# Optimization experiments

Measured on AMD Instinct MI355X. Metric: run time of the kernel, lower is better.

The kernel has to match this reference:

```python
import jax, jax.numpy as jnp
import numpy as np

QMIN, QMAX = -128, 127  # signed int8 range


def setup_inputs() -> dict:
    key = jax.random.key(0)
    k_x, k_w, k_b = jax.random.split(key, 3)
    N, C_in, H, W = 32, 128, 56, 56
    C_out, kH, kW = 256, 3, 3
    # int8-valued tensors carried as int32 (jax-friendly); values in [-128, 127]
    x = jax.random.randint(k_x, (N, C_in, H, W), 0, 256, dtype=jnp.int32) - 128
    weight = jax.random.randint(k_w, (C_out, C_in, kH, kW), 0, 256, dtype=jnp.int32) - 128
    # int32 bias, already quantized with scale s_in * s_w
    bias = jax.random.randint(k_b, (C_out,), -(2 ** 14), 2 ** 14, dtype=jnp.int32)
    return {
        "x": x,
        "weight": weight,
        "bias": bias,
        "input_scale": jnp.float32(0.02),
        "weight_scale": jnp.float32(0.005),
        "output_scale": jnp.float32(0.05),
        "input_zero_point": jnp.int32(-5),
        "output_zero_point": jnp.int32(3),
    }


def reference(x, weight, bias, input_scale, weight_scale, output_scale,
              input_zero_point, output_zero_point):
    # Dequant-style integer conv: shift input by its zero point (weights are
    # symmetric, zero point 0), accumulate in fp32 (stands in for int32 acc).
    x_f = (x - input_zero_point).astype(jnp.float32)
    w_f = weight.astype(jnp.float32)
    acc = jax.lax.conv_general_dilated(
        x_f, w_f,
        window_strides=(1, 1),
        padding=((1, 1), (1, 1)),
        dimension_numbers=("NCHW", "OIHW", "NCHW"),
    )
    acc = acc + bias.astype(jnp.float32)[None, :, None, None]
    # Requantize: scale fusion + output zero point, round, clamp to int8.
    requant_scale = input_scale * weight_scale / output_scale
    y = acc * requant_scale + output_zero_point.astype(jnp.float32)
    y_q = jnp.clip(jnp.round(y), QMIN, QMAX).astype(jnp.int8)
    return y_q
```

## Files before the change

### kernel.cpp

```cpp
#include <hip/hip_runtime.h>
#include <stdint.h>


#define NB 32
#define CI 128
#define HH 56
#define WW 56
#define CO 256
#define SPA (HH * WW)
#define HP 58
#define WP 64
#define XP2_BYTES (NB * HP * WP * CI)
#define BP_BYTES (9 * 2 * 4 * CO * 16)
#define ABUF (4 * 8192)

typedef int v4i __attribute__((ext_vector_type(4)));

__global__ __launch_bounds__(256) void prep_kernel(
    const int* __restrict__ x, const int* __restrict__ wgt,
    const int* __restrict__ bias, const int* __restrict__ zpi,
    int8_t* __restrict__ xp2, int8_t* __restrict__ bp, int* __restrict__ BG)
{
    __shared__ int sm[1824];
    const int tid = threadIdx.x, bid = blockIdx.x;
    const int zp = *zpi;
    const int zp4 = (zp & 255) * 0x01010101;

    if (bid < HH * NB) {
        const int n = bid / HH, h = bid % HH;
        #pragma unroll
        for (int it = 0; it < 7; ++it) {
            int j = tid + it * 256;
            int ci = j / 14, w4 = j - ci * 14;
            const v4i v = *(const v4i*)(x + ((n * CI + ci) * HH + h) * WW + w4 * 4);
            sm[w4 * 130 + ci] = (v.x & 255) | ((v.y & 255) << 8) |
                                ((v.z & 255) << 16) | (v.w << 24);
        }
        __syncthreads();
        int* od = (int*)xp2 + (n * HP + h + 1) * (WP * CI / 4);
        #pragma unroll
        for (int it = 0; it < 8; ++it) {
            int j = tid + it * 256;
            int widx = j >> 5, ci4 = j & 31;
            int val = zp4;
            if (widx >= 1 && widx <= WW) {
                int w = widx - 1;
                int base = (w >> 2) * 130 + ci4 * 4;
                int sh = (w & 3) * 8;
                val = ((sm[base] >> sh) & 0xff) | (((sm[base+1] >> sh) & 0xff) << 8) |
                      (((sm[base+2] >> sh) & 0xff) << 16) | ((sm[base+3] >> sh) << 24);
            }
            od[j ^ ((widx & 7) << 2)] = val;
        }
    } else if (bid < HH * NB + 2 * NB) {
        const int z = bid - HH * NB;
        const int n = z >> 1, hidx = (z & 1) ? (HP - 1) : 0;
        int* od = (int*)xp2 + (n * HP + hidx) * (WP * CI / 4);
        #pragma unroll
        for (int it = 0; it < 8; ++it) od[tid + it * 256] = zp4;
    } else {
        const int co = bid - (HH * NB + 2 * NB);
        for (int j = tid; j < 1152; j += 256) sm[j] = wgt[co * 1152 + j];
        __syncthreads();
        for (int j = tid; j < 288; j += 256) {
            int j4 = j & 3, q = (j >> 2) & 3, c64 = (j >> 4) & 1, t = j >> 5;
            int ci = c64 * 64 + q * 16 + j4 * 4;
            int b0 = sm[(ci + 0) * 9 + t] & 255, b1 = sm[(ci + 1) * 9 + t] & 255;
            int b2 = sm[(ci + 2) * 9 + t] & 255, b3 = sm[(ci + 3) * 9 + t];
            ((int*)bp)[((t * 2 + c64) * 4 + q) * 1024 + co * 4 + j4] =
                b0 | (b1 << 8) | (b2 << 16) | (b3 << 24);
        }
        if (tid < 9) {
            int s = 0;
            for (int ci = 0; ci < CI; ++ci) s += sm[ci * 9 + tid];
            sm[1152 + tid] = s;
        }
        __syncthreads();
        if (tid == 0) {
            int s9 = 0;
            for (int t = 0; t < 9; ++t) s9 += sm[1152 + t];
            BG[co] = bias[co] - zp * s9;
        }
    }
}

__global__ __launch_bounds__(256) void qconv_mfma(
    const int8_t* __restrict__ xp2, const int8_t* __restrict__ bp,
    const int* __restrict__ BG,
    const float* __restrict__ si, const float* __restrict__ sw,
    const float* __restrict__ so, const int* __restrict__ zpo,
    int* __restrict__ out)
{
    const int tid  = threadIdx.x, lane = tid & 63, wid = tid >> 6;
    const int quad = lane >> 4, lo16 = lane & 15;
    const int bid  = blockIdx.x;
    const int xcd  = bid & 7, idx = bid >> 3;
    const int n    = xcd * 4 + (idx & 3);
    const int cb   = (idx >> 2) & 1;
    const int s2   = idx >> 3;
    const int cw   = cb * 128 + wid * 32;

    __shared__ __attribute__((aligned(16))) int8_t Asm[ABUF];

    const int8_t* src0 = xp2 + (((size_t)n * HP + 2 * s2) << 13);
    #pragma unroll
    for (int k = 0; k < 8; ++k) {
        const int u = wid + 4 * k;
        __builtin_amdgcn_global_load_lds(
            (const __attribute__((address_space(1))) void*)(src0 + (u << 10) + lane * 16),
            (__attribute__((address_space(3))) void*)(&Asm[u << 10]), 16, 0, 0);
    }

    int bgv[2];
    #pragma unroll
    for (int ct = 0; ct < 2; ++ct) bgv[ct] = BG[cw + ct * 16 + lo16];
    const float rs = (*si) * (*sw) / (*so);
    const float zo = (float)(*zpo);

    int boff[7], sw3[7];
    #pragma unroll
    for (int mt = 0; mt < 7; ++mt) {
        const int ml = mt * 16 + lo16;
        const int srow = ml / 56, scol = ml - srow * 56;
        boff[mt] = srow * 8192 + scol * 128 + quad * 16;
        int t0 = ((scol + 0) & 7) << 4, t1 = ((scol + 1) & 7) << 4,
            t2 = ((scol + 2) & 7) << 4;
        sw3[mt] = t0 | (t1 << 8) | (t2 << 16);
    }

    const int8_t* bwav = bp + ((size_t)quad << 12) + ((cw + lo16) << 4);

    int* optr0 = out + ((size_t)n * CO + cw + lo16) * SPA + quad * 4;
    int* optr1 = optr0 + 16 * SPA;

    #define BLOAD(tp) {                                                        \
        const int8_t* bb = bwav + ((tp) * 8 << 12);                            \
        asm volatile("" : "+v"(bb));                                           \
        bt[tp][0] = *(const v4i*)(bb);                                         \
        bt[tp][1] = *(const v4i*)(bb + 256);                                   \
        bt[tp][2] = *(const v4i*)(bb + 16384);                                 \
        bt[tp][3] = *(const v4i*)(bb + 16384 + 256);                           \
    }

    #define AADDR(tp, mt) \
        ((boff[mt] + ((tp) / 3) * 8192 + ((tp) % 3) * 128) ^ \
         ((sw3[mt] >> (8 * ((tp) % 3))) & 0x70))

    v4i bt[9][4];
    BLOAD(0); BLOAD(1);

    v4i acc[7][2];
    #pragma unroll
    for (int mt = 0; mt < 7; ++mt) {
        acc[mt][0] = (v4i){0, 0, 0, 0};
        acc[mt][1] = (v4i){0, 0, 0, 0};
    }

    __syncthreads();

    v4i a0p[3], a1p[3];
    { const int p = AADDR(0, 0);
      a0p[0] = *(const v4i*)(Asm + p); a1p[0] = *(const v4i*)(Asm + (p ^ 64)); }
    { const int p = AADDR(0, 1);
      a0p[1] = *(const v4i*)(Asm + p); a1p[1] = *(const v4i*)(Asm + (p ^ 64)); }

    #pragma unroll
    for (int it = 0; it < 63; ++it) {
        const int tp = it / 7, mt = it % 7;
        if (mt == 0 && tp + 2 <= 8) BLOAD(tp + 2);
        if (it + 2 < 63) {
            const int tp2 = (it + 2) / 7, mt2 = (it + 2) % 7;
            const int p = AADDR(tp2, mt2);
            a0p[(it + 2) % 3] = *(const v4i*)(Asm + p);
            a1p[(it + 2) % 3] = *(const v4i*)(Asm + (p ^ 64));
        }
        const v4i a0 = a0p[it % 3], a1 = a1p[it % 3];
        acc[mt][0] = __builtin_amdgcn_mfma_i32_16x16x64_i8(a0, bt[tp][0], acc[mt][0], 0, 0, 0);
        acc[mt][1] = __builtin_amdgcn_mfma_i32_16x16x64_i8(a0, bt[tp][1], acc[mt][1], 0, 0, 0);
        acc[mt][0] = __builtin_amdgcn_mfma_i32_16x16x64_i8(a1, bt[tp][2], acc[mt][0], 0, 0, 0);
        acc[mt][1] = __builtin_amdgcn_mfma_i32_16x16x64_i8(a1, bt[tp][3], acc[mt][1], 0, 0, 0);
    }
    #undef BLOAD
    #undef AADDR

    const int m0 = s2 * 112;
    #pragma unroll
    for (int mt = 0; mt < 7; ++mt) {
        v4i v0, v1;
        #pragma unroll
        for (int i4 = 0; i4 < 4; ++i4) {
            float y0 = rintf((float)(acc[mt][0][i4] + bgv[0]) * rs + zo);
            float y1 = rintf((float)(acc[mt][1][i4] + bgv[1]) * rs + zo);
            v0[i4] = (int)fminf(fmaxf(y0, -128.f), 127.f);
            v1[i4] = (int)fminf(fmaxf(y1, -128.f), 127.f);
        }
        *(v4i*)(optr0 + m0 + mt * 16) = v0;
        *(v4i*)(optr1 + m0 + mt * 16) = v1;
    }
}

extern "C" void kernel_launch(void* const* d_in, const int* in_sizes, int n_in,
                              void* d_out, int out_size, void* d_ws, size_t ws_size,
                              hipStream_t stream) {
    const int*   x    = (const int*)d_in[0];
    const int*   wgt  = (const int*)d_in[1];
    const int*   bias = (const int*)d_in[2];
    const float* si   = (const float*)d_in[3];
    const float* sw   = (const float*)d_in[4];
    const float* so   = (const float*)d_in[5];
    const int*   zpi  = (const int*)d_in[6];
    const int*   zpo  = (const int*)d_in[7];
    int* out = (int*)d_out;

    int8_t* xp2 = (int8_t*)d_ws;
    int8_t* bp  = xp2 + XP2_BYTES;
    int*    bg  = (int*)(bp + BP_BYTES);

    prep_kernel<<<HH * NB + 2 * NB + CO, 256, 0, stream>>>(x, wgt, bias, zpi, xp2, bp, bg);
    qconv_mfma<<<1792, 256, 0, stream>>>(xp2, bp, bg, si, sw, so, zpo, out);
}
```

Measured before the change: 182.1 us.

## Widen per-block output channels to all 256, halving grid and reusing A tiles

Each block now computes all 256 output channels (64 per wave) for its spatial tile instead of 128, so the input tile staged in LDS is loaded once rather than twice and the grid drops from 1792 to 896 blocks. Accumulators double to 7x4 per wave and B fragments double to 8 per tap. The A and B prefetch distance shrinks from two steps ahead to one to offset the added register pressure. The larger register footprint may lower occupancy, and the smaller grid of 896 blocks gives less parallel slack across CUs.

```diff
diff --git a/kernel.cpp b/kernel.cpp
--- a/kernel.cpp
+++ b/kernel.cpp
@@ -96,9 +96,8 @@
     const int bid  = blockIdx.x;
     const int xcd  = bid & 7, idx = bid >> 3;
     const int n    = xcd * 4 + (idx & 3);
-    const int cb   = (idx >> 2) & 1;
-    const int s2   = idx >> 3;
-    const int cw   = cb * 128 + wid * 32;
+    const int s2   = idx >> 2;
+    const int cw   = wid * 64;
 
     __shared__ __attribute__((aligned(16))) int8_t Asm[ABUF];
 
@@ -111,9 +110,9 @@
             (__attribute__((address_space(3))) void*)(&Asm[u << 10]), 16, 0, 0);
     }
 
-    int bgv[2];
-    #pragma unroll
-    for (int ct = 0; ct < 2; ++ct) bgv[ct] = BG[cw + ct * 16 + lo16];
+    int bgv[4];
+    #pragma unroll
+    for (int ct = 0; ct < 4; ++ct) bgv[ct] = BG[cw + ct * 16 + lo16];
     const float rs = (*si) * (*sw) / (*so);
     const float zo = (float)(*zpo);
 
@@ -130,55 +129,57 @@
 
     const int8_t* bwav = bp + ((size_t)quad << 12) + ((cw + lo16) << 4);
 
-    int* optr0 = out + ((size_t)n * CO + cw + lo16) * SPA + quad * 4;
-    int* optr1 = optr0 + 16 * SPA;
+    int* optr = out + ((size_t)n * CO + cw + lo16) * SPA + quad * 4;
 
     #define BLOAD(tp) {                                                        \
         const int8_t* bb = bwav + ((tp) * 8 << 12);                            \
         asm volatile("" : "+v"(bb));                                           \
         bt[tp][0] = *(const v4i*)(bb);                                         \
         bt[tp][1] = *(const v4i*)(bb + 256);                                   \
-        bt[tp][2] = *(const v4i*)(bb + 16384);                                 \
-        bt[tp][3] = *(const v4i*)(bb + 16384 + 256);                           \
+        bt[tp][2] = *(const v4i*)(bb + 512);                                   \
+        bt[tp][3] = *(const v4i*)(bb + 768);                                   \
+        bt[tp][4] = *(const v4i*)(bb + 16384);                                 \
+        bt[tp][5] = *(const v4i*)(bb + 16384 + 256);                           \
+        bt[tp][6] = *(const v4i*)(bb + 16384 + 512);                           \
+        bt[tp][7] = *(const v4i*)(bb + 16384 + 768);                           \
     }
 
     #define AADDR(tp, mt) \
         ((boff[mt] + ((tp) / 3) * 8192 + ((tp) % 3) * 128) ^ \
          ((sw3[mt] >> (8 * ((tp) % 3))) & 0x70))
 
-    v4i bt[9][4];
-    BLOAD(0); BLOAD(1);
-
-    v4i acc[7][2];
-    #pragma unroll
-    for (int mt = 0; mt < 7; ++mt) {
-        acc[mt][0] = (v4i){0, 0, 0, 0};
-        acc[mt][1] = (v4i){0, 0, 0, 0};
-    }
+    v4i bt[9][8];
+    BLOAD(0);
+
+    v4i acc[7][4];
+    #pragma unroll
+    for (int mt = 0; mt < 7; ++mt)
+        #pragma unroll
+        for (int ct = 0; ct < 4; ++ct) acc[mt][ct] = (v4i){0, 0, 0, 0};
 
     __syncthreads();
 
-    v4i a0p[3], a1p[3];
+    v4i a0p[2], a1p[2];
     { const int p = AADDR(0, 0);
       a0p[0] = *(const v4i*)(Asm + p); a1p[0] = *(const v4i*)(Asm + (p ^ 64)); }
-    { const int p = AADDR(0, 1);
-      a0p[1] = *(const v4i*)(Asm + p); a1p[1] = *(const v4i*)(Asm + (p ^ 64)); }
 
     #pragma unroll
     for (int it = 0; it < 63; ++it) {
         const int tp = it / 7, mt = it % 7;
-        if (mt == 0 && tp + 2 <= 8) BLOAD(tp + 2);
-        if (it + 2 < 63) {
-            const int tp2 = (it + 2) / 7, mt2 = (it + 2) % 7;
-            const int p = AADDR(tp2, mt2);
-            a0p[(it + 2) % 3] = *(const v4i*)(Asm + p);
-            a1p[(it + 2) % 3] = *(const v4i*)(Asm + (p ^ 64));
-        }
-        const v4i a0 = a0p[it % 3], a1 = a1p[it % 3];
-        acc[mt][0] = __builtin_amdgcn_mfma_i32_16x16x64_i8(a0, bt[tp][0], acc[mt][0], 0, 0, 0);
-        acc[mt][1] = __builtin_amdgcn_mfma_i32_16x16x64_i8(a0, bt[tp][1], acc[mt][1], 0, 0, 0);
-        acc[mt][0] = __builtin_amdgcn_mfma_i32_16x16x64_i8(a1, bt[tp][2], acc[mt][0], 0, 0, 0);
-        acc[mt][1] = __builtin_amdgcn_mfma_i32_16x16x64_i8(a1, bt[tp][3], acc[mt][1], 0, 0, 0);
+        if (mt == 0 && tp + 1 <= 8) BLOAD(tp + 1);
+        if (it + 1 < 63) {
+            const int tp1 = (it + 1) / 7, mt1 = (it + 1) % 7;
+            const int p = AADDR(tp1, mt1);
+            a0p[(it + 1) & 1] = *(const v4i*)(Asm + p);
+            a1p[(it + 1) & 1] = *(const v4i*)(Asm + (p ^ 64));
+        }
+        const v4i a0 = a0p[it & 1], a1 = a1p[it & 1];
+        #pragma unroll
+        for (int ct = 0; ct < 4; ++ct)
+            acc[mt][ct] = __builtin_amdgcn_mfma_i32_16x16x64_i8(a0, bt[tp][ct], acc[mt][ct], 0, 0, 0);
+        #pragma unroll
+        for (int ct = 0; ct < 4; ++ct)
+            acc[mt][ct] = __builtin_amdgcn_mfma_i32_16x16x64_i8(a1, bt[tp][4 + ct], acc[mt][ct], 0, 0, 0);
     }
     #undef BLOAD
     #undef AADDR
@@ -186,16 +187,17 @@
     const int m0 = s2 * 112;
     #pragma unroll
     for (int mt = 0; mt < 7; ++mt) {
-        v4i v0, v1;
-        #pragma unroll
-        for (int i4 = 0; i4 < 4; ++i4) {
-            float y0 = rintf((float)(acc[mt][0][i4] + bgv[0]) * rs + zo);
-            float y1 = rintf((float)(acc[mt][1][i4] + bgv[1]) * rs + zo);
-            v0[i4] = (int)fminf(fmaxf(y0, -128.f), 127.f);
-            v1[i4] = (int)fminf(fmaxf(y1, -128.f), 127.f);
-        }
-        *(v4i*)(optr0 + m0 + mt * 16) = v0;
-        *(v4i*)(optr1 + m0 + mt * 16) = v1;
+        #pragma unroll
+        for (int ct = 0; ct < 4; ++ct) {
+            v4i vv;
+            #pragma unroll
+            for (int i4 = 0; i4 < 4; ++i4) {
+                float yv = rintf((float)(acc[mt][ct][i4] + bgv[ct]) * rs + zo);
+                yv = fminf(fmaxf(yv, -128.f), 127.f);
+                vv[i4] = (int)yv;
+            }
+            *(v4i*)(optr + ct * 16 * SPA + m0 + mt * 16) = vv;
+        }
     }
 }
 
@@ -217,5 +219,5 @@
     int*    bg  = (int*)(bp + BP_BYTES);
 
     prep_kernel<<<HH * NB + 2 * NB + CO, 256, 0, stream>>>(x, wgt, bias, zpi, xp2, bp, bg);
-    qconv_mfma<<<1792, 256, 0, stream>>>(xp2, bp, bg, si, sw, so, zpo, out);
+    qconv_mfma<<<896, 256, 0, stream>>>(xp2, bp, bg, si, sw, so, zpo, out);
 }
```

New measurement: 203.1 us. 11.6% more time.
